# Optimization experiments

Measured on AMD Instinct MI355X. Metric: run time of the kernel, lower is better.

Reference implementation:

```python
import jax, jax.numpy as jnp
import numpy as np

# ---- grid / frustum config (from default grid_config & data_config) ----
DB = (1.0, 60.0, 1.0)                 # dbound
OGH, OGW, DS = 256, 704, 16           # input size, downsample
FH, FW = OGH // DS, OGW // DS         # 16, 44
DEPTH = int(round((DB[1] - DB[0]) / DB[2]))  # 59 depth bins
NX0, NX1, NZ = 128, 128, 1            # BEV grid
DX = np.array([0.8, 0.8, 20.0], np.float32)
BX = np.array([-51.2 + 0.4, -51.2 + 0.4, 0.0], np.float32)  # row0 + dx/2


def _frustum():
    # (D, FH, FW, 3): pixel (u, v, depth)
    ds = jnp.broadcast_to(jnp.arange(DB[0], DB[1], DB[2], dtype=jnp.float32).reshape(-1, 1, 1), (DEPTH, FH, FW))
    xs = jnp.broadcast_to(jnp.linspace(0.0, OGW - 1.0, FW, dtype=jnp.float32).reshape(1, 1, FW), (DEPTH, FH, FW))
    ys = jnp.broadcast_to(jnp.linspace(0.0, OGH - 1.0, FH, dtype=jnp.float32).reshape(1, FH, 1), (DEPTH, FH, FW))
    return jnp.stack([xs, ys, ds], axis=-1)


def _geometry(rots, trans, intrins, post_rots, post_trans, bda):
    # pixel frustum -> ego-frame 3D points; (B, N, D, FH, FW, 3)
    pts = _frustum() - post_trans[:, :, None, None, None, :]
    pts = jnp.einsum('bnij,bndhwj->bndhwi', jnp.linalg.inv(post_rots), pts)
    pts = jnp.concatenate([pts[..., :2] * pts[..., 2:3], pts[..., 2:3]], axis=-1)
    comb = jnp.einsum('bnij,bnjk->bnik', rots, jnp.linalg.inv(intrins))
    pts = jnp.einsum('bnij,bndhwj->bndhwi', comb, pts) + trans[:, :, None, None, None, :]
    pts = jnp.einsum('bij,bndhwj->bndhwi', bda, pts)
    return pts


def _voxel_pool(geom, vol):
    # geom: (B,N,D,FH,FW,3), vol: (B,N,D,FH,FW,C) -> BEV (B, C*NZ, NX0, NX1)
    B, C = vol.shape[0], vol.shape[-1]
    gidx = jnp.floor((geom - (BX - DX / 2.0)) / DX).astype(jnp.int32)
    kept = ((gidx[..., 0] >= 0) & (gidx[..., 0] < NX0)
            & (gidx[..., 1] >= 0) & (gidx[..., 1] < NX1)
            & (gidx[..., 2] >= 0) & (gidx[..., 2] < NZ))
    bidx = jnp.broadcast_to(jnp.arange(B, dtype=jnp.int32).reshape(B, 1, 1, 1, 1), gidx.shape[:-1])
    flat = ((bidx * NZ + gidx[..., 2]) * NX0 + gidx[..., 0]) * NX1 + gidx[..., 1]
    nvox = B * NZ * NX0 * NX1
    flat = jnp.where(kept, flat, nvox).reshape(-1)      # dump bucket for culled pts
    feats = vol.reshape(-1, C)
    bev = jax.ops.segment_sum(feats, flat, num_segments=nvox + 1)[:nvox]
    bev = bev.reshape(B, NZ, NX0, NX1, C)
    bev = jnp.moveaxis(bev, -1, 2).reshape(B, NZ * C, NX0, NX1)  # z-major channel cat
    return bev


def setup_inputs() -> dict:
    key = jax.random.key(0)
    B, N, CIN, CT = 4, 6, 512, 64
    k1, k2 = jax.random.split(key, 2)
    x = jax.random.normal(k1, (B, N, CIN, FH, FW), dtype=jnp.float32)
    weight = jax.random.normal(k2, (DEPTH + CT, CIN), dtype=jnp.float32) * 0.02
    bias = jnp.zeros((DEPTH + CT,), dtype=jnp.float32)
    # cam->ego rotation (cam z forward -> ego x, cam x right -> ego -y, cam y down -> ego -z)
    Rcam = jnp.asarray(np.array([[0., 0., 1.], [-1., 0., 0.], [0., -1., 0.]], np.float32))
    rots = jnp.tile(Rcam, (B, N, 1, 1))
    trans = jnp.zeros((B, N, 3), dtype=jnp.float32)
    K = jnp.asarray(np.array([[600., 0., 352.], [0., 600., 128.], [0., 0., 1.]], np.float32))
    intrins = jnp.tile(K, (B, N, 1, 1))
    post_rots = jnp.tile(jnp.eye(3, dtype=jnp.float32), (B, N, 1, 1))
    post_trans = jnp.zeros((B, N, 3), dtype=jnp.float32)
    bda = jnp.tile(jnp.eye(3, dtype=jnp.float32), (B, 1, 1))
    return dict(x=x, rots=rots, trans=trans, intrins=intrins, post_rots=post_rots,
                post_trans=post_trans, bda=bda, weight=weight, bias=bias)


def reference(x, rots, trans, intrins, post_rots, post_trans, bda, weight, bias):
    # 1x1 depth/context head (eval mode): (B,N,Cin,H,W) -> (B,N,D+C,H,W)
    out = jnp.einsum('bnchw,oc->bnohw', x, weight) + bias[None, None, :, None, None]
    depth = jax.nn.softmax(out[:, :, :DEPTH], axis=2)      # (B,N,D,H,W)
    feat = out[:, :, DEPTH:]                               # (B,N,C,H,W)
    # depth-context outer product -> frustum volume (B,N,D,H,W,C)
    vol = jnp.einsum('bndhw,bnchw->bndhwc', depth, feat)
    geom = _geometry(rots, trans, intrins, post_rots, post_trans, bda)
    bev = _voxel_pool(geom, vol)                           # (B, C*NZ, 128, 128)
    return bev, depth
```

## Files before the change

kernel.cpp:

```cpp
#include <hip/hip_runtime.h>
#include <math.h>

#define CIN   512
#define NOUT  123
#define DEPN  59
#define CT    64
#define B_    4
#define N_    6
#define FH    16
#define FW    44
#define HW    704
#define NPIX  (B_*N_*HW)
#define NX    128
#define BEV_ELEMS (B_*CT*NX*NX)
#define DEPTH_OFF BEV_ELEMS

#define TDREC   40
#define WS_WB   1920
#define WS_PS   (WS_WB + 32768)
#define WS_FS   (WS_PS + NPIX*64)
#define WS_GC   (WS_FS + NPIX*64)

typedef short bf16x8 __attribute__((ext_vector_type(8)));
typedef float f32x4  __attribute__((ext_vector_type(4)));

__device__ inline unsigned short f2bf(float f) {
    unsigned u = __float_as_uint(f);
    return (unsigned short)((u + 0x7fffu + ((u >> 16) & 1u)) >> 16);
}

__device__ inline void inv3d(const double* m, double* o) {
    #pragma clang fp contract(off)
    double c00 = m[4]*m[8] - m[5]*m[7];
    double c01 = m[5]*m[6] - m[3]*m[8];
    double c02 = m[3]*m[7] - m[4]*m[6];
    double det = m[0]*c00 + m[1]*c01 + m[2]*c02;
    o[0] = c00/det; o[1] = (m[2]*m[7]-m[1]*m[8])/det; o[2] = (m[1]*m[5]-m[2]*m[4])/det;
    o[3] = c01/det; o[4] = (m[0]*m[8]-m[2]*m[6])/det; o[5] = (m[2]*m[3]-m[0]*m[5])/det;
    o[6] = c02/det; o[7] = (m[1]*m[6]-m[0]*m[7])/det; o[8] = (m[0]*m[4]-m[1]*m[3])/det;
}
__device__ inline void mm3d(const double* a, const double* b, double* o) {
    #pragma clang fp contract(off)
    for (int i = 0; i < 3; ++i)
        for (int k = 0; k < 3; ++k)
            o[i*3+k] = (a[i*3+0]*b[0*3+k] + a[i*3+1]*b[1*3+k]) + a[i*3+2]*b[2*3+k];
}

__global__ void k0_prep(const float* __restrict__ rots, const float* __restrict__ trans,
                        const float* __restrict__ intr, const float* __restrict__ prots,
                        const float* __restrict__ ptrans, const float* __restrict__ bda,
                        const float* __restrict__ W, float* __restrict__ ws,
                        float* __restrict__ dout) {
    int tid = blockIdx.x * 256 + threadIdx.x;
    int stride = gridDim.x * 256;
    float4 z = {0.f, 0.f, 0.f, 0.f};
    for (int i = tid; i < BEV_ELEMS / 4; i += stride)
        *(float4*)(dout + 4 * (size_t)i) = z;
    unsigned short* wb = (unsigned short*)(ws + WS_WB);
    for (int i = tid; i < 128 * CIN; i += stride) {
        int o = i >> 9, c = i & 511;
        wb[i] = (o < NOUT) ? f2bf(W[o * CIN + c]) : (unsigned short)0;
    }
    if (blockIdx.x == 0 && threadIdx.x < B_ * N_) {
        #pragma clang fp contract(off)
        int t = threadIdx.x;
        int b = t / N_;
        double* X = (double*)(ws) + t * TDREC;
        double PR[9], Kd[9], Rd[9], Bd[9];
        for (int i = 0; i < 9; ++i) PR[i] = (double)prots[t * 9 + i];
        for (int i = 0; i < 9; ++i) Kd[i] = (double)intr[t * 9 + i];
        for (int i = 0; i < 9; ++i) Rd[i] = (double)rots[t * 9 + i];
        for (int i = 0; i < 9; ++i) Bd[i] = (double)bda[b * 9 + i];
        double iPR[9]; inv3d(PR, iPR);
        for (int i = 0; i < 9; ++i) X[i] = iPR[i];
        for (int i = 0; i < 3; ++i) X[9 + i] = (double)ptrans[t * 3 + i];
        double iK[9];  inv3d(Kd, iK);
        double comb[9]; mm3d(Rd, iK, comb);
        for (int i = 0; i < 9; ++i) X[12 + i] = comb[i];
        for (int i = 0; i < 3; ++i) X[21 + i] = (double)trans[t * 3 + i];
        for (int i = 0; i < 9; ++i) X[24 + i] = Bd[i];
    }
}

__global__ __launch_bounds__(256) void k0b_coef(float* __restrict__ ws) {
    #pragma clang fp contract(off)
    int i = blockIdx.x * 256 + threadIdx.x;
    int b = i / (FW * 96);
    int rem = i - b * (FW * 96);
    int w = rem / 96;
    int j = rem - w * 96;
    int n = j >> 4, h = j & 15;
    const double* T = (const double*)(ws) + (b * N_ + n) * TDREC;
    const double xs = (w == 43) ? 703.0 : (double)w * (703.0 / 43.0);
    const double ys = (double)(h * 17);
    const double u0 = xs - T[9];
    const double u1 = ys - T[10];
    double pA[3], pB[3];
    #pragma unroll
    for (int k = 0; k < 3; ++k) {
        pA[k] = (T[3*k]*u0 + T[3*k+1]*u1) - T[3*k+2]*T[11];
        pB[k] = T[3*k+2];
    }
    double q0c[3] = { pA[0]*pA[2], pA[0]*pB[2] + pB[0]*pA[2], pB[0]*pB[2] };
    double q1c[3] = { pA[1]*pA[2], pA[1]*pB[2] + pB[1]*pA[2], pB[1]*pB[2] };
    double q2c[3] = { pA[2], pB[2], 0.0 };
    double rc[3][3], gc[3][3];
    #pragma unroll
    for (int r = 0; r < 3; ++r)
        #pragma unroll
        for (int k = 0; k < 3; ++k)
            rc[r][k] = ((T[12+3*r]*q0c[k] + T[13+3*r]*q1c[k]) + T[14+3*r]*q2c[k])
                       + ((k == 0) ? T[21+r] : 0.0);
    #pragma unroll
    for (int g = 0; g < 3; ++g)
        #pragma unroll
        for (int k = 0; k < 3; ++k)
            gc[g][k] = (T[24+3*g]*rc[0][k] + T[25+3*g]*rc[1][k]) + T[26+3*g]*rc[2][k];
    double* dst = (double*)(ws) + WS_GC / 2 + (size_t)i * 9;
    #pragma unroll
    for (int t = 0; t < 9; ++t) dst[t] = gc[t / 3][t % 3];
}

#define K1A   (64 * 72)
#define K1T   (K1A + 128 * 72)
__global__ __launch_bounds__(512) void k1_gemm(const float* __restrict__ x,
                                               const float* __restrict__ bias,
                                               float* __restrict__ ws,
                                               float* __restrict__ dout) {
    __shared__ __align__(16) unsigned short smem[2][2][K1T];
    const int tid = threadIdx.x;
    const int grp = tid >> 8;
    const int gtid = tid & 255;
    const int wave = gtid >> 6;
    const int lane = tid & 63;
    const int l15 = lane & 15, quad = lane >> 4;
    const int bn = blockIdx.y;
    const int pixbase = blockIdx.x * 64;
    const float* xg = x + (size_t)bn * CIN * HW + pixbase;
    const unsigned short* wbg = (const unsigned short*)(ws + WS_WB);
    const int cpack = gtid >> 4;
    const int pix4 = (gtid & 15) * 4;
    const int wo  = gtid >> 3;
    const int wsub = gtid & 7;
    const int ck0 = grp * 256;

    f32x4 acc[8] = {};
    float4 r0, r1, r2, r3;
    uint4  w4[4];

    {
        const float* src = xg + (size_t)(ck0 + 4 * cpack) * HW + pix4;
        r0 = *(const float4*)(src);
        r1 = *(const float4*)(src + HW);
        r2 = *(const float4*)(src + 2 * HW);
        r3 = *(const float4*)(src + 3 * HW);
        #pragma unroll
        for (int i = 0; i < 4; ++i)
            w4[i] = *(const uint4*)(wbg + (size_t)(wo + 32 * i) * CIN + ck0 + wsub * 8);
    }

    #pragma unroll
    for (int it = 0; it < 4; ++it) {
        const int buf = it & 1;
        unsigned short* sa = smem[grp][buf];
        unsigned short* sb = smem[grp][buf] + K1A;
        {
            const float* f0 = (const float*)&r0; const float* f1 = (const float*)&r1;
            const float* f2 = (const float*)&r2; const float* f3 = (const float*)&r3;
            #pragma unroll
            for (int i = 0; i < 4; ++i) {
                uint2 pk;
                pk.x = (unsigned)f2bf(f0[i]) | ((unsigned)f2bf(f1[i]) << 16);
                pk.y = (unsigned)f2bf(f2[i]) | ((unsigned)f2bf(f3[i]) << 16);
                *(uint2*)&sa[(pix4 + i) * 72 + 4 * cpack] = pk;
            }
            #pragma unroll
            for (int i = 0; i < 4; ++i)
                *(uint4*)&sb[(wo + 32 * i) * 72 + wsub * 8] = w4[i];
        }
        if (it < 3) {
            const int ck = ck0 + (it + 1) * 64;
            const float* src = xg + (size_t)(ck + 4 * cpack) * HW + pix4;
            r0 = *(const float4*)(src);
            r1 = *(const float4*)(src + HW);
            r2 = *(const float4*)(src + 2 * HW);
            r3 = *(const float4*)(src + 3 * HW);
            #pragma unroll
            for (int i = 0; i < 4; ++i)
                w4[i] = *(const uint4*)(wbg + (size_t)(wo + 32 * i) * CIN + ck + wsub * 8);
        }
        __syncthreads();
        #pragma unroll
        for (int ks = 0; ks < 64; ks += 32) {
            const bf16x8 a = *(const bf16x8*)&sa[(wave * 16 + l15) * 72 + ks + quad * 8];
            #pragma unroll
            for (int nt = 0; nt < 8; ++nt) {
                const bf16x8 b = *(const bf16x8*)&sb[(nt * 16 + l15) * 72 + ks + quad * 8];
                acc[nt] = __builtin_amdgcn_mfma_f32_16x16x32_bf16(a, b, acc[nt], 0, 0, 0);
            }
        }
    }

    __syncthreads();
    float* red = (float*)&smem[0][0][0];
    if (grp == 1) {
        #pragma unroll
        for (int nt = 0; nt < 8; ++nt)
            #pragma unroll
            for (int reg = 0; reg < 4; ++reg)
                red[(wave * 16 + quad * 4 + reg) * 132 + nt * 16 + l15] = acc[nt][reg];
    }
    __syncthreads();
    if (grp == 0) {
        #pragma unroll
        for (int nt = 0; nt < 8; ++nt)
            #pragma unroll
            for (int reg = 0; reg < 4; ++reg)
                acc[nt][reg] += red[(wave * 16 + quad * 4 + reg) * 132 + nt * 16 + l15];
    }
    __syncthreads();

    float* sred = (float*)&smem[0][0][0];
    const int b = bn / N_, n = bn - b * N_;
    if (grp == 0) {
        float bb[8];
        #pragma unroll
        for (int nt = 0; nt < 8; ++nt) {
            int o = nt * 16 + l15;
            bb[nt] = (o < NOUT) ? bias[o] : 0.0f;
        }
        float* ps = ws + WS_PS;
        float* fs = ws + WS_FS;
        #pragma unroll
        for (int reg = 0; reg < 4; ++reg) {
            int pixl = wave * 16 + quad * 4 + reg;
            int pix = pixbase + pixl;
            int h = pix / FW, w = pix - h * FW;
            size_t row = (size_t)(b * FW + w) * 96 + n * FH + h;
            float v[4]; float m = -INFINITY;
            #pragma unroll
            for (int nt = 0; nt < 4; ++nt) {
                v[nt] = acc[nt][reg] + bb[nt];
                if (nt * 16 + l15 < DEPN) m = fmaxf(m, v[nt]);
            }
            #pragma unroll
            for (int msk = 8; msk >= 1; msk >>= 1) m = fmaxf(m, __shfl_xor(m, msk, 64));
            float e[4], s = 0.0f;
            #pragma unroll
            for (int nt = 0; nt < 4; ++nt) {
                e[nt] = (nt * 16 + l15 < DEPN) ? expf(v[nt] - m) : 0.0f;
                s += e[nt];
            }
            #pragma unroll
            for (int msk = 8; msk >= 1; msk >>= 1) s += __shfl_xor(s, msk, 64);
            const float inv = 1.0f / s;
            #pragma unroll
            for (int nt = 0; nt < 4; ++nt) {
                int o = nt * 16 + l15;
                if (o < DEPN) {
                    float p = e[nt] * inv;
                    ps[row * 64 + o] = p;
                    sred[pixl * 65 + o] = p;
                } else fs[row * 64 + (o - DEPN)] = v[nt];
            }
            #pragma unroll
            for (int nt = 4; nt < 8; ++nt) {
                int o = nt * 16 + l15;
                if (o < NOUT) fs[row * 64 + (o - DEPN)] = acc[nt][reg] + bb[nt];
            }
        }
    }
    __syncthreads();
    const int wv8 = tid >> 6;
    for (int o = wv8; o < DEPN; o += 8)
        dout[DEPTH_OFF + ((size_t)bn * DEPN + o) * HW + pixbase + lane] = sred[lane * 65 + o];
}

#define DQ2 16
__global__ __launch_bounds__(256) void k2b_geom(float* __restrict__ ws,
                                                float* __restrict__ dout) {
    __shared__ float sF[96][64];
    __shared__ float sP[DQ2][100];
    __shared__ unsigned short sv16[DQ2 * 96];
    __shared__ __align__(16) double sG[96 * 9];
    __shared__ int sflag[DQ2];
    const int tid = threadIdx.x;
    const int bw = blockIdx.x;
    const int b = bw / FW;
    const int dbase = blockIdx.y * DQ2;
    const int nd = min(DQ2, DEPN - dbase);

    {
        const float* fsrc = ws + WS_FS + (size_t)bw * (96 * 64);
        const float* psrc = ws + WS_PS + (size_t)bw * (96 * 64);
        for (int i = tid; i < 96 * 16; i += 256) {
            int j = i >> 4, c4 = (i & 15) * 4;
            *(float4*)&sF[j][c4] = *(const float4*)(fsrc + j * 64 + c4);
        }
        for (int i = tid; i < 96 * 4; i += 256) {
            int j = i >> 2, q = i & 3;
            const float4 p4 = *(const float4*)(psrc + j * 64 + dbase + 4 * q);
            sP[4 * q + 0][j] = p4.x; sP[4 * q + 1][j] = p4.y;
            sP[4 * q + 2][j] = p4.z; sP[4 * q + 3][j] = p4.w;
        }
        const double2* gsrc = (const double2*)((const double*)(ws) + WS_GC / 2
                                               + (size_t)bw * (96 * 9));
        for (int i = tid; i < 432; i += 256)
            ((double2*)sG)[i] = gsrc[i];
    }
    __syncthreads();

    {
        const double BXY = (double)(-51.2000007629394531f);
        for (int idx = tid; idx < nd * 96; idx += 256) {
            int dl = idx / 96, j = idx - dl * 96;
            const double* G = &sG[j * 9];
            const double dsv = (double)(dbase + dl + 1);
            const double g0 = (G[2] * dsv + G[1]) * dsv + G[0];
            const double g1 = (G[5] * dsv + G[4]) * dsv + G[3];
            const double g2 = (G[8] * dsv + G[7]) * dsv + G[6];
            const double fx = floor((g0 - BXY) * 1.25);
            const double fy = floor((g1 - BXY) * 1.25);
            const bool keep = (fx >= 0.0) & (fx < 128.0) & (fy >= 0.0) & (fy < 128.0) &
                              (g2 >= -10.0) & (g2 < 10.0);
            sv16[idx] = keep ? (unsigned short)((int)fx * NX + (int)fy) : (unsigned short)0xFFFF;
        }
    }
    __syncthreads();

    {
        const int dl = tid >> 4, s = tid & 15;
        int u = -1, mix = 0;
        const int base = dl * 96 + s * 6;
        #pragma unroll
        for (int t = 0; t < 6; ++t) {
            int v = sv16[base + t];
            if (v != 0xFFFF) { if (u < 0) u = v; else if (v != u) mix = 1; }
        }
        #pragma unroll
        for (int msk = 1; msk < 16; msk <<= 1) {
            int uo = __shfl_xor(u, msk, 64);
            int mo = __shfl_xor(mix, msk, 64);
            mix = mix | mo | ((u >= 0 && uo >= 0 && uo != u) ? 1 : 0);
            u = (u < 0) ? uo : u;
        }
        if (s == 0 && dl < nd) sflag[dl] = mix ? -2 : u;
    }
    for (int idx = tid; idx < nd * 96; idx += 256) {
        if (sv16[idx] == 0xFFFF) {
            int dl = idx / 96, j = idx - dl * 96;
            sP[dl][j] = 0.0f;
        }
    }
    __syncthreads();

    const int dl = tid >> 4, ci = tid & 15;
    if (dl < nd && sflag[dl] >= 0) {
        float ax = 0.f, ay = 0.f, az = 0.f, aw = 0.f;
        for (int jj = 0; jj < 96; jj += 4) {
            const float4 pv = *(const float4*)&sP[dl][jj];
            const float4 f0 = *(const float4*)&sF[jj + 0][4 * ci];
            const float4 f1 = *(const float4*)&sF[jj + 1][4 * ci];
            const float4 f2 = *(const float4*)&sF[jj + 2][4 * ci];
            const float4 f3 = *(const float4*)&sF[jj + 3][4 * ci];
            ax = fmaf(pv.x, f0.x, ax); ay = fmaf(pv.x, f0.y, ay);
            az = fmaf(pv.x, f0.z, az); aw = fmaf(pv.x, f0.w, aw);
            ax = fmaf(pv.y, f1.x, ax); ay = fmaf(pv.y, f1.y, ay);
            az = fmaf(pv.y, f1.z, az); aw = fmaf(pv.y, f1.w, aw);
            ax = fmaf(pv.z, f2.x, ax); ay = fmaf(pv.z, f2.y, ay);
            az = fmaf(pv.z, f2.z, az); aw = fmaf(pv.z, f2.w, aw);
            ax = fmaf(pv.w, f3.x, ax); ay = fmaf(pv.w, f3.y, ay);
            az = fmaf(pv.w, f3.z, az); aw = fmaf(pv.w, f3.w, aw);
        }
        float* dst = dout + (((size_t)(b * CT + 4 * ci)) << 14) + sflag[dl];
        atomicAdd(dst,             ax);
        atomicAdd(dst + (1 << 14), ay);
        atomicAdd(dst + (2 << 14), az);
        atomicAdd(dst + (3 << 14), aw);
    }
    for (int d2 = 0; d2 < nd; ++d2) {
        if (sflag[d2] == -2) {
            int c = tid & 63, g = tid >> 6;
            for (int jj = 0; jj < 24; ++jj) {
                int j = g * 24 + jj;
                int v = sv16[d2 * 96 + j];
                if (v != 0xFFFF)
                    atomicAdd(dout + (((size_t)(b * CT + c)) << 14) + v,
                              sP[d2][j] * sF[j][c]);
            }
        }
    }
}

extern "C" void kernel_launch(void* const* d_in, const int* in_sizes, int n_in,
                              void* d_out, int out_size, void* d_ws, size_t ws_size,
                              hipStream_t stream) {
    const float* x      = (const float*)d_in[0];
    const float* rots   = (const float*)d_in[1];
    const float* trans  = (const float*)d_in[2];
    const float* intr   = (const float*)d_in[3];
    const float* prots  = (const float*)d_in[4];
    const float* ptrans = (const float*)d_in[5];
    const float* bda    = (const float*)d_in[6];
    const float* W      = (const float*)d_in[7];
    const float* bias   = (const float*)d_in[8];
    float* out = (float*)d_out;
    float* ws  = (float*)d_ws;

    k0_prep<<<512, 256, 0, stream>>>(rots, trans, intr, prots, ptrans, bda, W, ws, out);
    k0b_coef<<<66, 256, 0, stream>>>(ws);
    k1_gemm<<<dim3(HW / 64, B_ * N_), 512, 0, stream>>>(x, bias, ws, out);
    k2b_geom<<<dim3(B_ * FW, 4), 256, 0, stream>>>(ws, out);
}
```

Before: 161.1 us.

## Drop split-K in projection GEMM; use 256-thread blocks with two-deep register prefetch

The 1x1 projection GEMM kernel no longer splits the 512-channel reduction across two 256-thread groups. A single 256-thread group now walks all 8 K-chunks, prefetching two chunks ahead in registers. This removes the shared-memory cross-group reduction and its extra barriers, and allows two blocks per CU. The cost is half as many threads per block issuing loads and MFMAs, a longer serial K loop, and more registers held by the doubled prefetch buffers.

```diff
diff --git a/kernel.cpp b/kernel.cpp
--- a/kernel.cpp
+++ b/kernel.cpp
@@ -123,50 +123,50 @@
 
 #define K1A   (64 * 72)
 #define K1T   (K1A + 128 * 72)
-__global__ __launch_bounds__(512) void k1_gemm(const float* __restrict__ x,
-                                               const float* __restrict__ bias,
-                                               float* __restrict__ ws,
-                                               float* __restrict__ dout) {
-    __shared__ __align__(16) unsigned short smem[2][2][K1T];
+__global__ __launch_bounds__(256, 2) void k1_gemm(const float* __restrict__ x,
+                                                  const float* __restrict__ bias,
+                                                  float* __restrict__ ws,
+                                                  float* __restrict__ dout) {
+    __shared__ __align__(16) unsigned short smem[2][K1T];
     const int tid = threadIdx.x;
-    const int grp = tid >> 8;
-    const int gtid = tid & 255;
-    const int wave = gtid >> 6;
-    const int lane = tid & 63;
+    const int wave = tid >> 6, lane = tid & 63;
     const int l15 = lane & 15, quad = lane >> 4;
     const int bn = blockIdx.y;
     const int pixbase = blockIdx.x * 64;
     const float* xg = x + (size_t)bn * CIN * HW + pixbase;
     const unsigned short* wbg = (const unsigned short*)(ws + WS_WB);
-    const int cpack = gtid >> 4;
-    const int pix4 = (gtid & 15) * 4;
-    const int wo  = gtid >> 3;
-    const int wsub = gtid & 7;
-    const int ck0 = grp * 256;
+    const int cpack = tid >> 4;
+    const int pix4 = (tid & 15) * 4;
+    const int wo  = tid >> 3;
+    const int wsub = tid & 7;
 
     f32x4 acc[8] = {};
-    float4 r0, r1, r2, r3;
-    uint4  w4[4];
-
-    {
-        const float* src = xg + (size_t)(ck0 + 4 * cpack) * HW + pix4;
-        r0 = *(const float4*)(src);
-        r1 = *(const float4*)(src + HW);
-        r2 = *(const float4*)(src + 2 * HW);
-        r3 = *(const float4*)(src + 3 * HW);
+    float4 xr[2][4];
+    uint4  wr[2][4];
+
+    #pragma unroll
+    for (int d = 0; d < 2; ++d) {
+        const int ck = d * 64;
+        const float* src = xg + (size_t)(ck + 4 * cpack) * HW + pix4;
+        xr[d][0] = *(const float4*)(src);
+        xr[d][1] = *(const float4*)(src + HW);
+        xr[d][2] = *(const float4*)(src + 2 * HW);
+        xr[d][3] = *(const float4*)(src + 3 * HW);
         #pragma unroll
         for (int i = 0; i < 4; ++i)
-            w4[i] = *(const uint4*)(wbg + (size_t)(wo + 32 * i) * CIN + ck0 + wsub * 8);
-    }
-
-    #pragma unroll
-    for (int it = 0; it < 4; ++it) {
+            wr[d][i] = *(const uint4*)(wbg + (size_t)(wo + 32 * i) * CIN + ck + wsub * 8);
+    }
+
+    #pragma unroll
+    for (int it = 0; it < 8; ++it) {
         const int buf = it & 1;
-        unsigned short* sa = smem[grp][buf];
-        unsigned short* sb = smem[grp][buf] + K1A;
+        unsigned short* sa = smem[buf];
+        unsigned short* sb = smem[buf] + K1A;
         {
-            const float* f0 = (const float*)&r0; const float* f1 = (const float*)&r1;
-            const float* f2 = (const float*)&r2; const float* f3 = (const float*)&r3;
+            const float* f0 = (const float*)&xr[buf][0];
+            const float* f1 = (const float*)&xr[buf][1];
+            const float* f2 = (const float*)&xr[buf][2];
+            const float* f3 = (const float*)&xr[buf][3];
             #pragma unroll
             for (int i = 0; i < 4; ++i) {
                 uint2 pk;
@@ -176,18 +176,18 @@
             }
             #pragma unroll
             for (int i = 0; i < 4; ++i)
-                *(uint4*)&sb[(wo + 32 * i) * 72 + wsub * 8] = w4[i];
-        }
-        if (it < 3) {
-            const int ck = ck0 + (it + 1) * 64;
+                *(uint4*)&sb[(wo + 32 * i) * 72 + wsub * 8] = wr[buf][i];
+        }
+        if (it < 6) {
+            const int ck = (it + 2) * 64;
             const float* src = xg + (size_t)(ck + 4 * cpack) * HW + pix4;
-            r0 = *(const float4*)(src);
-            r1 = *(const float4*)(src + HW);
-            r2 = *(const float4*)(src + 2 * HW);
-            r3 = *(const float4*)(src + 3 * HW);
+            xr[buf][0] = *(const float4*)(src);
+            xr[buf][1] = *(const float4*)(src + HW);
+            xr[buf][2] = *(const float4*)(src + 2 * HW);
+            xr[buf][3] = *(const float4*)(src + 3 * HW);
             #pragma unroll
             for (int i = 0; i < 4; ++i)
-                w4[i] = *(const uint4*)(wbg + (size_t)(wo + 32 * i) * CIN + ck + wsub * 8);
+                wr[buf][i] = *(const uint4*)(wbg + (size_t)(wo + 32 * i) * CIN + ck + wsub * 8);
         }
         __syncthreads();
         #pragma unroll
@@ -201,28 +201,9 @@
         }
     }
 
-    __syncthreads();
-    float* red = (float*)&smem[0][0][0];
-    if (grp == 1) {
-        #pragma unroll
-        for (int nt = 0; nt < 8; ++nt)
-            #pragma unroll
-            for (int reg = 0; reg < 4; ++reg)
-                red[(wave * 16 + quad * 4 + reg) * 132 + nt * 16 + l15] = acc[nt][reg];
-    }
-    __syncthreads();
-    if (grp == 0) {
-        #pragma unroll
-        for (int nt = 0; nt < 8; ++nt)
-            #pragma unroll
-            for (int reg = 0; reg < 4; ++reg)
-                acc[nt][reg] += red[(wave * 16 + quad * 4 + reg) * 132 + nt * 16 + l15];
-    }
-    __syncthreads();
-
-    float* sred = (float*)&smem[0][0][0];
+    float* sred = (float*)&smem[0][0];
     const int b = bn / N_, n = bn - b * N_;
-    if (grp == 0) {
+    {
         float bb[8];
         #pragma unroll
         for (int nt = 0; nt < 8; ++nt) {
@@ -271,8 +252,7 @@
         }
     }
     __syncthreads();
-    const int wv8 = tid >> 6;
-    for (int o = wv8; o < DEPN; o += 8)
+    for (int o = wave; o < DEPN; o += 4)
         dout[DEPTH_OFF + ((size_t)bn * DEPN + o) * HW + pixbase + lane] = sred[lane * 65 + o];
 }
 
@@ -409,6 +389,6 @@
 
     k0_prep<<<512, 256, 0, stream>>>(rots, trans, intr, prots, ptrans, bda, W, ws, out);
     k0b_coef<<<66, 256, 0, stream>>>(ws);
-    k1_gemm<<<dim3(HW / 64, B_ * N_), 512, 0, stream>>>(x, bias, ws, out);
+    k1_gemm<<<dim3(HW / 64, B_ * N_), 256, 0, stream>>>(x, bias, ws, out);
     k2b_geom<<<dim3(B_ * FW, 4), 256, 0, stream>>>(ws, out);
 }
```

New measurement: 163.0 us. No clear change (+1.2%).
